# Kernel optimization log

Measured on AMD Instinct MI355X. Metric: run time of the kernel, lower is better.

## Reference

```python
import jax, jax.numpy as jnp
import numpy as np

N = 100000

def gcn_conv(x, src, dst, norm, W, b, num_nodes):
    # x: [N, Cin] -> [N, Cout]; GCNConv: linear transform then normalized sum aggregation
    h = x @ W                                   # [N, Cout]
    msg = h[src] * norm[:, None]                # [E+N, Cout] gather + scale
    out = jax.ops.segment_sum(msg, dst, num_segments=num_nodes)  # scatter-add
    return out + b

def _norm_coeffs(src, dst, num_nodes):
    # symmetric normalization D^{-1/2} A_hat D^{-1/2} with self-loops already in src/dst
    deg = jax.ops.segment_sum(jnp.ones_like(src, dtype=jnp.float32), dst, num_segments=num_nodes)
    dinv = jnp.where(deg > 0, jax.lax.rsqrt(jnp.maximum(deg, 1.0)), 0.0)
    return dinv[src] * dinv[dst]

def setup_inputs() -> dict:
    key = jax.random.key(0)
    ks = jax.random.split(key, 8)
    Cin, Ch, Cout, E = 128, 128, 47, 1600000
    x = jax.random.normal(ks[0], (N, Cin), dtype=jnp.float32)
    edge_index = jax.random.randint(ks[1], (2, E), 0, N, dtype=jnp.int64)
    def glorot(k, fan_in, fan_out):
        s = jnp.sqrt(6.0 / (fan_in + fan_out))
        return jax.random.uniform(k, (fan_in, fan_out), jnp.float32, -s, s)
    return {
        'x': x, 'edge_index': edge_index,
        'W1': glorot(ks[2], Cin, Ch), 'b1': jnp.zeros((Ch,), jnp.float32),
        'W2': glorot(ks[3], Ch, Ch),  'b2': jnp.zeros((Ch,), jnp.float32),
        'W3': glorot(ks[4], Ch, Cout),'b3': jnp.zeros((Cout,), jnp.float32),
    }

def reference(x, edge_index, W1, b1, W2, b2, W3, b3):
    num_nodes = x.shape[0]
    loop = jnp.arange(num_nodes, dtype=edge_index.dtype)
    src = jnp.concatenate([edge_index[0], loop])
    dst = jnp.concatenate([edge_index[1], loop])
    norm = _norm_coeffs(src, dst, num_nodes)
    # eval-mode forward: dropout(p=0.5, training=False) is identity
    h = gcn_conv(x, src, dst, norm, W1, b1, num_nodes)
    h = jax.nn.relu(h)
    h = gcn_conv(h, src, dst, norm, W2, b2, num_nodes)
    h = jax.nn.relu(h)
    h = gcn_conv(h, src, dst, norm, W3, b3, num_nodes)
    return jax.nn.log_softmax(h, axis=1)
```

## Files before the change

### kernel.cpp

```cpp
#include <hip/hip_runtime.h>
#include <stdint.h>

typedef __bf16 bf16x8 __attribute__((ext_vector_type(8)));
typedef float f32x4 __attribute__((ext_vector_type(4)));

#define CHB 8192

__device__ __forceinline__ float bf2f(unsigned short s) {
    union { unsigned u; float f; } x; x.u = ((unsigned)s) << 16; return x.f;
}
__device__ __forceinline__ unsigned short f2bf(float f) {
    union { float f; unsigned u; } x; x.f = f;
    unsigned r = x.u + 0x7fffu + ((x.u >> 16) & 1u);
    return (unsigned short)(r >> 16);
}

__global__ __launch_bounds__(256) void k_hist(const int* __restrict__ dst, int E, int nPB,
                                              int* __restrict__ bhist, int NB) {
    __shared__ int h[256];
    int t = threadIdx.x;
    h[t] = 0;
    __syncthreads();
    int blk = blockIdx.x;
    int hi = min((blk + 1) * CHB, E);
    for (int e = blk * CHB + t; e < hi; e += 256) atomicAdd(&h[dst[e] >> 9], 1);
    __syncthreads();
    if (t < NB) bhist[t * nPB + blk] = h[t];
}

__global__ __launch_bounds__(256) void k_scan_part(const int* __restrict__ deg,
                                                   int* __restrict__ part, int N) {
    __shared__ int wsum[4];
    int t = threadIdx.x;
    int lane = t & 63, wv = t >> 6;
    int base = blockIdx.x * 1024 + t * 4;
    int s = 0;
#pragma unroll
    for (int j = 0; j < 4; ++j) {
        int i = base + j;
        if (i < N) s += deg[i];
    }
    for (int off = 1; off < 64; off <<= 1) s += __shfl_xor(s, off, 64);
    if (lane == 0) wsum[wv] = s;
    __syncthreads();
    if (t == 0) part[blockIdx.x] = wsum[0] + wsum[1] + wsum[2] + wsum[3];
}

__global__ void k_scan_mid(int* __restrict__ part, int nb) {
    __shared__ int buf[256];
    int t = threadIdx.x;
    buf[t] = (t < nb) ? part[t] : 0;
    __syncthreads();
    for (int off = 1; off < 256; off <<= 1) {
        int v = buf[t];
        int u = (t >= off) ? buf[t - off] : 0;
        __syncthreads();
        buf[t] = v + u;
        __syncthreads();
    }
    if (t < nb) part[t] = (t == 0) ? 0 : buf[t - 1];
}

__global__ __launch_bounds__(256) void k_scan_final(const int* __restrict__ deg,
                                                    const int* __restrict__ part,
                                                    int* __restrict__ out, int N) {
    __shared__ int wsum[4];
    int t = threadIdx.x;
    int lane = t & 63, wv = t >> 6;
    int base = blockIdx.x * 1024 + t * 4;
    int v[4];
    int s = 0;
#pragma unroll
    for (int j = 0; j < 4; ++j) {
        int i = base + j;
        v[j] = (i < N) ? deg[i] : 0;
        s += v[j];
    }
    int inc = s;
    for (int off = 1; off < 64; off <<= 1) {
        int u = __shfl_up(inc, off, 64);
        if (lane >= off) inc += u;
    }
    if (lane == 63) wsum[wv] = inc;
    __syncthreads();
    int excl = part[blockIdx.x] + inc - s;
    for (int w = 0; w < wv; ++w) excl += wsum[w];
#pragma unroll
    for (int j = 0; j < 4; ++j) {
        int i = base + j;
        if (i < N) {
            out[i] = excl;
            excl += v[j];
            if (i == N - 1) out[N] = excl;
        }
    }
}

__global__ __launch_bounds__(256) void k_partition(const int* __restrict__ src,
                                                   const int* __restrict__ dst, int E,
                                                   int nPB, const int* __restrict__ bscan,
                                                   unsigned* __restrict__ part_edges, int NB) {
    __shared__ int cur[256];
    int t = threadIdx.x;
    int blk = blockIdx.x;
    if (t < NB) cur[t] = bscan[t * nPB + blk];
    __syncthreads();
    int hi = min((blk + 1) * CHB, E);
    for (int e = blk * CHB + t; e < hi; e += 256) {
        int d = dst[e];
        int s = src[e];
        int pos = atomicAdd(&cur[d >> 9], 1);
        part_edges[pos] = ((unsigned)(d & 511) << 17) | (unsigned)s;
    }
}

__global__ __launch_bounds__(256) void k_bucket(const unsigned* __restrict__ part_edges,
                                                const int* __restrict__ bscan, int nPB,
                                                int N, int Npad, int* __restrict__ row_ptr,
                                                float* __restrict__ dinv,
                                                int* __restrict__ ssrc) {
    __shared__ int cnt[512];
    __shared__ int excl[512];
    __shared__ int wsum[4];
    int t = threadIdx.x;
    int b = blockIdx.x;
    int pb = bscan[b * nPB];
    int pe = bscan[(b + 1) * nPB];
    cnt[t] = 0; cnt[t + 256] = 0;
    __syncthreads();
    for (int e = pb + t; e < pe; e += 256)
        atomicAdd(&cnt[(part_edges[e] >> 17) & 511], 1);
    __syncthreads();
    int a0 = cnt[2 * t], a1 = cnt[2 * t + 1];
    int s = a0 + a1;
    int lane = t & 63, wv = t >> 6;
    int inc = s;
    for (int off = 1; off < 64; off <<= 1) {
        int u = __shfl_up(inc, off, 64);
        if (lane >= off) inc += u;
    }
    if (lane == 63) wsum[wv] = inc;
    __syncthreads();
    int pre = inc - s;
    for (int w = 0; w < wv; ++w) pre += wsum[w];
    excl[2 * t] = pre;
    excl[2 * t + 1] = pre + a0;
    int base = b << 9;
#pragma unroll
    for (int j = 0; j < 2; ++j) {
        int i = 2 * t + j;
        int g = base + i;
        int c = (j == 0) ? a0 : a1;
        int ex = (j == 0) ? pre : pre + a0;
        if (g < N) {
            row_ptr[g] = pb + ex;
            if (g == N - 1) row_ptr[N] = pb + ex + c;
        }
        if (g < Npad) dinv[g] = rsqrtf((float)c + 1.0f);
    }
    __syncthreads();
    for (int e = pb + t; e < pe; e += 256) {
        unsigned pk = part_edges[e];
        int doff = (pk >> 17) & 511;
        int pos = pb + atomicAdd(&excl[doff], 1);
        ssrc[pos] = (int)(pk & 0x1FFFFu);
    }
}

__global__ void k_cvt_x(const float4* __restrict__ x, ushort4* __restrict__ out, int n4) {
    int i = blockIdx.x * blockDim.x + threadIdx.x;
    if (i < n4) {
        float4 v = x[i];
        ushort4 o;
        o.x = f2bf(v.x); o.y = f2bf(v.y); o.z = f2bf(v.z); o.w = f2bf(v.w);
        out[i] = o;
    }
}

__global__ void k_wfrag(const float* __restrict__ W, unsigned short* __restrict__ Wf,
                        int Ncol, int realCols) {
    int NT = Ncol >> 4;
    int total = 4 * NT * 64 * 8;
    int idx = blockIdx.x * blockDim.x + threadIdx.x;
    if (idx >= total) return;
    int j = idx & 7;
    int l = (idx >> 3) & 63;
    int t = idx >> 9;
    int n = t % NT;
    int kk = t / NT;
    int k = kk * 32 + ((l >> 4) << 3) + j;
    int c = (n << 4) + (l & 15);
    float v = (c < realCols) ? W[k * realCols + c] : 0.0f;
    Wf[idx] = f2bf(v);
}

template<int NT>
__global__ __launch_bounds__(256) void k_gemm(const unsigned short* __restrict__ A,
                                              const unsigned short* __restrict__ Wf,
                                              const float* __restrict__ dinv,
                                              unsigned short* __restrict__ Hout) {
    int lane = threadIdx.x & 63;
    int wv = threadIdx.x >> 6;
    int rb = blockIdx.x * 4 + wv;
    size_t row0 = (size_t)rb * 16;
    const unsigned short* arow = A + (row0 + (lane & 15)) * 128 + ((lane >> 4) << 3);
    f32x4 acc[NT];
#pragma unroll
    for (int n = 0; n < NT; ++n) acc[n] = (f32x4){0.f, 0.f, 0.f, 0.f};
#pragma unroll
    for (int kk = 0; kk < 4; ++kk) {
        bf16x8 a = *(const bf16x8*)(arow + kk * 32);
#pragma unroll
        for (int n = 0; n < NT; ++n) {
            bf16x8 b = *(const bf16x8*)(Wf + (((kk * NT + n) * 64 + lane) << 3));
            acc[n] = __builtin_amdgcn_mfma_f32_16x16x32_bf16(a, b, acc[n], 0, 0, 0);
        }
    }
    const int NCOL = NT * 16;
    size_t crow = row0 + ((lane >> 4) << 2);
    int ccol = lane & 15;
    float dv[4];
#pragma unroll
    for (int q = 0; q < 4; ++q) dv[q] = dinv[crow + q];
#pragma unroll
    for (int n = 0; n < NT; ++n) {
#pragma unroll
        for (int q = 0; q < 4; ++q) {
            Hout[(crow + q) * NCOL + n * 16 + ccol] = f2bf(acc[n][q] * dv[q]);
        }
    }
}

__global__ __launch_bounds__(256) void k_agg(const unsigned short* __restrict__ H,
                                             const int* __restrict__ row_ptr,
                                             const int* __restrict__ ssrc,
                                             const float* __restrict__ dinv,
                                             const float* __restrict__ bias,
                                             unsigned short* __restrict__ Out, int N) {
    int lane = threadIdx.x & 63;
    int i = blockIdx.x * 4 + (threadIdx.x >> 6);
    if (i >= N) return;
    float dv = dinv[i];
    unsigned v = *(const unsigned*)(H + ((size_t)i << 7) + (lane << 1));
    float acc0 = bf2f((unsigned short)(v & 0xffff));
    float acc1 = bf2f((unsigned short)(v >> 16));
    int e = row_ptr[i], e1 = row_ptr[i + 1];
#pragma unroll 4
    for (; e < e1; ++e) {
        int s = ssrc[e];
        unsigned hv = *(const unsigned*)(H + ((size_t)s << 7) + (lane << 1));
        acc0 += bf2f((unsigned short)(hv & 0xffff));
        acc1 += bf2f((unsigned short)(hv >> 16));
    }
    acc0 = fmaxf(acc0 * dv + bias[lane * 2], 0.f);
    acc1 = fmaxf(acc1 * dv + bias[lane * 2 + 1], 0.f);
    unsigned o = (unsigned)f2bf(acc0) | ((unsigned)f2bf(acc1) << 16);
    *(unsigned*)(Out + ((size_t)i << 7) + (lane << 1)) = o;
}

__global__ __launch_bounds__(256) void k_agg3(const unsigned short* __restrict__ H,
                                              const int* __restrict__ row_ptr,
                                              const int* __restrict__ ssrc,
                                              const float* __restrict__ dinv,
                                              const float* __restrict__ b3,
                                              float* __restrict__ Out, int N, int Cout) {
    int lane = threadIdx.x & 63;
    int i = blockIdx.x * 4 + (threadIdx.x >> 6);
    if (i >= N) return;
    float dv = dinv[i];
    float acc = bf2f(H[((size_t)i << 6) + lane]);
    int e = row_ptr[i], e1 = row_ptr[i + 1];
#pragma unroll 4
    for (; e < e1; ++e) {
        int s = ssrc[e];
        acc += bf2f(H[((size_t)s << 6) + lane]);
    }
    float z = (lane < Cout) ? acc * dv + b3[lane] : -1e30f;
    float m = z;
    for (int off = 32; off; off >>= 1) m = fmaxf(m, __shfl_xor(m, off, 64));
    float p = (lane < Cout) ? expf(z - m) : 0.f;
    float ssum = p;
    for (int off = 32; off; off >>= 1) ssum += __shfl_xor(ssum, off, 64);
    if (lane < Cout) Out[(size_t)i * Cout + lane] = z - m - logf(ssum);
}

extern "C" void kernel_launch(void* const* d_in, const int* in_sizes, int n_in,
                              void* d_out, int out_size, void* d_ws, size_t ws_size,
                              hipStream_t stream) {
    const float* x  = (const float*)d_in[0];
    const int*   ei = (const int*)d_in[1];
    const float* W1 = (const float*)d_in[2];
    const float* b1 = (const float*)d_in[3];
    const float* W2 = (const float*)d_in[4];
    const float* b2 = (const float*)d_in[5];
    const float* W3 = (const float*)d_in[6];
    const float* b3 = (const float*)d_in[7];

    const int N = in_sizes[0] / 128;
    const int E = in_sizes[1] / 2;
    const int Cout = in_sizes[7];
    const int Npad = (N + 63) & ~63;
    const int* srcp = ei;
    const int* dstp = ei + E;

    const int NB  = (N + 511) >> 9;
    const int nPB = (E + CHB - 1) / CHB;
    const int M   = NB * nPB;

    char* p = (char*)d_ws;
    auto alloc = [&](size_t bytes) -> void* {
        void* r = (void*)p;
        p += (bytes + 255) & ~(size_t)255;
        return r;
    };
    float* dinv     = (float*)alloc((size_t)Npad * 4);
    int*   row_ptr  = (int*)alloc((size_t)(N + 1) * 4);
    int*   bhist    = (int*)alloc((size_t)M * 4);
    int*   bscan    = (int*)alloc((size_t)(M + 1) * 4);
    int*   part     = (int*)alloc(1024 * 4);
    unsigned* pedge = (unsigned*)alloc((size_t)E * 4);
    int*   ssrc     = (int*)alloc((size_t)E * 4);
    unsigned short* xb  = (unsigned short*)alloc((size_t)Npad * 128 * 2);
    unsigned short* hb  = (unsigned short*)alloc((size_t)Npad * 128 * 2);
    unsigned short* ab  = (unsigned short*)alloc((size_t)Npad * 128 * 2);
    unsigned short* wf1 = (unsigned short*)alloc(128 * 128 * 2);
    unsigned short* wf2 = (unsigned short*)alloc(128 * 128 * 2);
    unsigned short* wf3 = (unsigned short*)alloc(128 * 64 * 2);

    const int nb2 = (M + 1023) / 1024;
    k_hist<<<nPB, 256, 0, stream>>>(dstp, E, nPB, bhist, NB);
    k_scan_part<<<nb2, 256, 0, stream>>>(bhist, part, M);
    k_scan_mid<<<1, 256, 0, stream>>>(part, nb2);
    k_scan_final<<<nb2, 256, 0, stream>>>(bhist, part, bscan, M);
    k_partition<<<nPB, 256, 0, stream>>>(srcp, dstp, E, nPB, bscan, pedge, NB);
    k_bucket<<<NB, 256, 0, stream>>>(pedge, bscan, nPB, N, Npad, row_ptr, dinv, ssrc);

    k_cvt_x<<<(N * 128 / 4 + 255) / 256, 256, 0, stream>>>((const float4*)x, (ushort4*)xb,
                                                           N * 128 / 4);
    k_wfrag<<<(16384 + 255) / 256, 256, 0, stream>>>(W1, wf1, 128, 128);
    k_wfrag<<<(16384 + 255) / 256, 256, 0, stream>>>(W2, wf2, 128, 128);
    k_wfrag<<<(8192 + 255) / 256, 256, 0, stream>>>(W3, wf3, 64, Cout);

    const int gemmGrid = Npad / 64;
    const int aggGrid = (N + 3) / 4;

    k_gemm<8><<<gemmGrid, 256, 0, stream>>>(xb, wf1, dinv, hb);
    k_agg<<<aggGrid, 256, 0, stream>>>(hb, row_ptr, ssrc, dinv, b1, ab, N);
    k_gemm<8><<<gemmGrid, 256, 0, stream>>>(ab, wf2, dinv, hb);
    k_agg<<<aggGrid, 256, 0, stream>>>(hb, row_ptr, ssrc, dinv, b2, ab, N);
    k_gemm<4><<<gemmGrid, 256, 0, stream>>>(ab, wf3, dinv, hb);
    k_agg3<<<aggGrid, 256, 0, stream>>>(hb, row_ptr, ssrc, dinv, b3,
                                        (float*)d_out, N, Cout);
}
```

Before: 331.5 us.

## Split aggregation wavefront into edge groups with 16-byte vector gathers

The aggregation kernels now split each 64-lane wavefront into sub-groups that each handle a different edge, and every lane loads 16 bytes (8 bf16 channels) per edge instead of 4 or 2 bytes. Source indices are fetched cooperatively 64 at a time and broadcast with shuffles, and partial sums are combined across groups with xor-shuffles. This raises memory-level parallelism and cuts the number of load instructions in the latency-bound gather loop. The costs are extra cross-lane reduction work, lanes left idle on the tail of each row, and a log-softmax epilogue that is now computed per 8-channel chunk.

```diff
diff --git a/kernel.cpp b/kernel.cpp
--- a/kernel.cpp
+++ b/kernel.cpp
@@ -8,6 +8,9 @@
 
 __device__ __forceinline__ float bf2f(unsigned short s) {
     union { unsigned u; float f; } x; x.u = ((unsigned)s) << 16; return x.f;
+}
+__device__ __forceinline__ float bitf(unsigned u) {
+    union { unsigned u; float f; } x; x.u = u; return x.f;
 }
 __device__ __forceinline__ unsigned short f2bf(float f) {
     union { float f; unsigned u; } x; x.f = f;
@@ -240,22 +243,59 @@
     int lane = threadIdx.x & 63;
     int i = blockIdx.x * 4 + (threadIdx.x >> 6);
     if (i >= N) return;
-    float dv = dinv[i];
-    unsigned v = *(const unsigned*)(H + ((size_t)i << 7) + (lane << 1));
-    float acc0 = bf2f((unsigned short)(v & 0xffff));
-    float acc1 = bf2f((unsigned short)(v >> 16));
-    int e = row_ptr[i], e1 = row_ptr[i + 1];
-#pragma unroll 4
-    for (; e < e1; ++e) {
-        int s = ssrc[e];
-        unsigned hv = *(const unsigned*)(H + ((size_t)s << 7) + (lane << 1));
-        acc0 += bf2f((unsigned short)(hv & 0xffff));
-        acc1 += bf2f((unsigned short)(hv >> 16));
-    }
-    acc0 = fmaxf(acc0 * dv + bias[lane * 2], 0.f);
-    acc1 = fmaxf(acc1 * dv + bias[lane * 2 + 1], 0.f);
-    unsigned o = (unsigned)f2bf(acc0) | ((unsigned)f2bf(acc1) << 16);
-    *(unsigned*)(Out + ((size_t)i << 7) + (lane << 1)) = o;
+    int g = lane >> 4;
+    int c16 = lane & 15;
+    const uint4* Hv = (const uint4*)H;
+    float acc[8];
+#pragma unroll
+    for (int c = 0; c < 8; ++c) acc[c] = 0.f;
+    int e0 = row_ptr[i], e1 = row_ptr[i + 1];
+    for (int base = e0; base < e1; base += 64) {
+        int cnt = min(64, e1 - base);
+        int sidx = (lane < cnt) ? ssrc[base + lane] : 0;
+        for (int j = 0; j < cnt; j += 4) {
+            int jj = j + g;
+            int s = __shfl(sidx, jj, 64);
+            if (jj < cnt) {
+                uint4 v = Hv[((size_t)s << 4) + c16];
+                acc[0] += bitf(v.x << 16); acc[1] += bitf(v.x & 0xffff0000u);
+                acc[2] += bitf(v.y << 16); acc[3] += bitf(v.y & 0xffff0000u);
+                acc[4] += bitf(v.z << 16); acc[5] += bitf(v.z & 0xffff0000u);
+                acc[6] += bitf(v.w << 16); acc[7] += bitf(v.w & 0xffff0000u);
+            }
+        }
+    }
+    if (g == 0) {
+        uint4 v = Hv[((size_t)i << 4) + c16];
+        acc[0] += bitf(v.x << 16); acc[1] += bitf(v.x & 0xffff0000u);
+        acc[2] += bitf(v.y << 16); acc[3] += bitf(v.y & 0xffff0000u);
+        acc[4] += bitf(v.z << 16); acc[5] += bitf(v.z & 0xffff0000u);
+        acc[6] += bitf(v.w << 16); acc[7] += bitf(v.w & 0xffff0000u);
+    }
+#pragma unroll
+    for (int c = 0; c < 8; ++c) {
+        acc[c] += __shfl_xor(acc[c], 16, 64);
+        acc[c] += __shfl_xor(acc[c], 32, 64);
+    }
+    if (g == 0) {
+        float dv = dinv[i];
+        const float4* bv = (const float4*)bias;
+        float4 b0 = bv[c16 * 2], b1 = bv[c16 * 2 + 1];
+        float r0 = fmaxf(acc[0] * dv + b0.x, 0.f);
+        float r1 = fmaxf(acc[1] * dv + b0.y, 0.f);
+        float r2 = fmaxf(acc[2] * dv + b0.z, 0.f);
+        float r3 = fmaxf(acc[3] * dv + b0.w, 0.f);
+        float r4 = fmaxf(acc[4] * dv + b1.x, 0.f);
+        float r5 = fmaxf(acc[5] * dv + b1.y, 0.f);
+        float r6 = fmaxf(acc[6] * dv + b1.z, 0.f);
+        float r7 = fmaxf(acc[7] * dv + b1.w, 0.f);
+        uint4 o;
+        o.x = (unsigned)f2bf(r0) | ((unsigned)f2bf(r1) << 16);
+        o.y = (unsigned)f2bf(r2) | ((unsigned)f2bf(r3) << 16);
+        o.z = (unsigned)f2bf(r4) | ((unsigned)f2bf(r5) << 16);
+        o.w = (unsigned)f2bf(r6) | ((unsigned)f2bf(r7) << 16);
+        ((uint4*)Out)[((size_t)i << 4) + c16] = o;
+    }
 }
 
 __global__ __launch_bounds__(256) void k_agg3(const unsigned short* __restrict__ H,
@@ -267,21 +307,66 @@
     int lane = threadIdx.x & 63;
     int i = blockIdx.x * 4 + (threadIdx.x >> 6);
     if (i >= N) return;
+    int g = lane >> 3;
+    int c8 = lane & 7;
+    const uint4* Hv = (const uint4*)H;
+    float acc[8];
+#pragma unroll
+    for (int c = 0; c < 8; ++c) acc[c] = 0.f;
+    int e0 = row_ptr[i], e1 = row_ptr[i + 1];
+    for (int base = e0; base < e1; base += 64) {
+        int cnt = min(64, e1 - base);
+        int sidx = (lane < cnt) ? ssrc[base + lane] : 0;
+        for (int j = 0; j < cnt; j += 8) {
+            int jj = j + g;
+            int s = __shfl(sidx, jj, 64);
+            if (jj < cnt) {
+                uint4 v = Hv[((size_t)s << 3) + c8];
+                acc[0] += bitf(v.x << 16); acc[1] += bitf(v.x & 0xffff0000u);
+                acc[2] += bitf(v.y << 16); acc[3] += bitf(v.y & 0xffff0000u);
+                acc[4] += bitf(v.z << 16); acc[5] += bitf(v.z & 0xffff0000u);
+                acc[6] += bitf(v.w << 16); acc[7] += bitf(v.w & 0xffff0000u);
+            }
+        }
+    }
+    if (g == 0) {
+        uint4 v = Hv[((size_t)i << 3) + c8];
+        acc[0] += bitf(v.x << 16); acc[1] += bitf(v.x & 0xffff0000u);
+        acc[2] += bitf(v.y << 16); acc[3] += bitf(v.y & 0xffff0000u);
+        acc[4] += bitf(v.z << 16); acc[5] += bitf(v.z & 0xffff0000u);
+        acc[6] += bitf(v.w << 16); acc[7] += bitf(v.w & 0xffff0000u);
+    }
+#pragma unroll
+    for (int c = 0; c < 8; ++c) {
+        acc[c] += __shfl_xor(acc[c], 8, 64);
+        acc[c] += __shfl_xor(acc[c], 16, 64);
+        acc[c] += __shfl_xor(acc[c], 32, 64);
+    }
     float dv = dinv[i];
-    float acc = bf2f(H[((size_t)i << 6) + lane]);
-    int e = row_ptr[i], e1 = row_ptr[i + 1];
-#pragma unroll 4
-    for (; e < e1; ++e) {
-        int s = ssrc[e];
-        acc += bf2f(H[((size_t)s << 6) + lane]);
-    }
-    float z = (lane < Cout) ? acc * dv + b3[lane] : -1e30f;
-    float m = z;
-    for (int off = 32; off; off >>= 1) m = fmaxf(m, __shfl_xor(m, off, 64));
-    float p = (lane < Cout) ? expf(z - m) : 0.f;
-    float ssum = p;
-    for (int off = 32; off; off >>= 1) ssum += __shfl_xor(ssum, off, 64);
-    if (lane < Cout) Out[(size_t)i * Cout + lane] = z - m - logf(ssum);
+    float z[8];
+    float m = -1e30f;
+#pragma unroll
+    for (int c = 0; c < 8; ++c) {
+        int ch = c8 * 8 + c;
+        z[c] = (ch < Cout) ? acc[c] * dv + b3[ch] : -1e30f;
+        m = fmaxf(m, z[c]);
+    }
+    for (int off = 1; off < 8; off <<= 1) m = fmaxf(m, __shfl_xor(m, off, 64));
+    float ssum = 0.f;
+#pragma unroll
+    for (int c = 0; c < 8; ++c) {
+        int ch = c8 * 8 + c;
+        if (ch < Cout) ssum += expf(z[c] - m);
+    }
+    for (int off = 1; off < 8; off <<= 1) ssum += __shfl_xor(ssum, off, 64);
+    if (g == 0) {
+        float lg = m + logf(ssum);
+#pragma unroll
+        for (int c = 0; c < 8; ++c) {
+            int ch = c8 * 8 + c;
+            if (ch < Cout) Out[(size_t)i * Cout + ch] = z[c] - lg;
+        }
+    }
 }
 
 extern "C" void kernel_launch(void* const* d_in, const int* in_sizes, int n_in,
```

Result: no change. 330.2 us (-0.4%).
